# Kernel optimization log

Measured on AMD Instinct MI355X. Metric: run time of the kernel, lower is better.

## Reference

```python
import jax, jax.numpy as jnp
import numpy as np

N = 49152   # nodes (1024 graphs * 48 teeth)
G = 1024    # graphs
E = 65536   # edges per relation
H, C, R = 8, 48, 3
FUSED = 384
NEG = 0.2   # RGATConv negative_slope default
EPS = 1e-5


def _ln_global(x, w, b):
    # PyG LayerNorm mode='graph' with batch=None: normalize over ALL elements
    x = x - jnp.mean(x)
    return x / (jnp.std(x) + EPS) * w + b


def _ln_graph(x, batch, w, b):
    # PyG LayerNorm mode='graph' with batch: per-graph mean/var over nodes+features
    f = x.shape[-1]
    cnt = jnp.maximum(jax.ops.segment_sum(jnp.ones((x.shape[0],), x.dtype), batch, num_segments=G), 1.0) * f
    mean = jax.ops.segment_sum(x, batch, num_segments=G).sum(-1) / cnt  # [G]
    xc = x - mean[batch][:, None]
    var = jax.ops.segment_sum(xc * xc, batch, num_segments=G).sum(-1) / cnt
    return xc / jnp.sqrt(var + EPS)[batch][:, None] * w + b


def _rgat(x, src, dst, etype, W, q, k, b):
    # RGATConv: per-relation transform, additive self-attention, across-relation segment softmax
    xt = jnp.einsum('nf,rfc->rnc', x, W)          # [R,N,H*C] transform once per relation
    oi = xt[etype, dst]                            # [E,H*C] destination (x_i) transformed
    oj = xt[etype, src]                            # [E,H*C] source (x_j) transformed
    alpha = jax.nn.leaky_relu(oi @ q + oj @ k, NEG)   # [E,H]
    m = jax.lax.stop_gradient(jax.ops.segment_max(alpha, dst, num_segments=N))
    a = jnp.exp(alpha - m[dst])
    s = jax.ops.segment_sum(a, dst, num_segments=N)
    a = a / (s[dst] + 1e-16)                       # segment softmax over in-edges per head
    msg = (a[:, :, None] * oj.reshape(-1, H, C)).reshape(-1, H * C)
    return jax.ops.segment_sum(msg, dst, num_segments=N) + b


def _enc(x, w, b, lw, lb):
    return _ln_global(jax.nn.relu(x @ w + b), lw, lb)


def _forward(floats, ei_o, ei_a, ei_s, batch):
    (x_visual, x_geom, x_prior, vis_w, vis_b, vis_lw, vis_lb, geom_w, geom_b, geom_lw, geom_lb,
     prior_w, prior_b, prior_lw, prior_lb, r1_w, r1_q, r1_k, r1_b, n1_w, n1_b,
     r2_w, r2_q, r2_k, r2_b, n2_w, n2_b, c_w1, c_b1, c_w2, c_b2) = floats
    ei = jnp.concatenate([ei_o, ei_a, ei_s], axis=1)
    etype = jnp.concatenate([jnp.zeros((ei_o.shape[1],), jnp.int32),
                             jnp.ones((ei_a.shape[1],), jnp.int32),
                             jnp.full((ei_s.shape[1],), 2, jnp.int32)])
    src, dst = ei[0], ei[1]
    h0 = jnp.concatenate([_enc(x_visual, vis_w, vis_b, vis_lw, vis_lb),
                          _enc(x_geom, geom_w, geom_b, geom_lw, geom_lb),
                          _enc(x_prior, prior_w, prior_b, prior_lw, prior_lb)], axis=-1)
    h1 = _ln_graph(h0 + jax.nn.elu(_rgat(h0, src, dst, etype, r1_w, r1_q, r1_k, r1_b)), batch, n1_w, n1_b)
    h2 = _ln_graph(h1 + jax.nn.elu(_rgat(h1, src, dst, etype, r2_w, r2_q, r2_k, r2_b)), batch, n2_w, n2_b)
    return jax.nn.relu(h2 @ c_w1 + c_b1) @ c_w2 + c_b2


def setup_inputs() -> dict:
    key = jax.random.key(0)
    ks = jax.random.split(key, 20)
    def rn(i, shape, s=0.05):
        return jax.random.normal(ks[i], shape, jnp.float32) * s
    return dict(
        x_visual=rn(0, (N, 1024), 1.0),
        x_geom=rn(1, (N, 6), 1.0),
        x_prior=rn(2, (N, 50), 1.0),
        vis_w=rn(3, (1024, 128)), vis_b=jnp.zeros((128,)), vis_lw=jnp.ones((128,)), vis_lb=jnp.zeros((128,)),
        geom_w=rn(4, (6, 128)), geom_b=jnp.zeros((128,)), geom_lw=jnp.ones((128,)), geom_lb=jnp.zeros((128,)),
        prior_w=rn(5, (50, 128)), prior_b=jnp.zeros((128,)), prior_lw=jnp.ones((128,)), prior_lb=jnp.zeros((128,)),
        r1_w=rn(6, (R, FUSED, H * C)), r1_q=rn(7, (H * C, H)), r1_k=rn(8, (H * C, H)), r1_b=jnp.zeros((H * C,)),
        n1_w=jnp.ones((FUSED,)), n1_b=jnp.zeros((FUSED,)),
        r2_w=rn(9, (R, FUSED, H * C)), r2_q=rn(10, (H * C, H)), r2_k=rn(11, (H * C, H)), r2_b=jnp.zeros((H * C,)),
        n2_w=jnp.ones((FUSED,)), n2_b=jnp.zeros((FUSED,)),
        c_w1=rn(12, (FUSED, 128)), c_b1=jnp.zeros((128,)), c_w2=rn(13, (128, 49)), c_b2=jnp.zeros((49,)),
        edge_index_overlap=jax.random.randint(ks[14], (2, E), 0, N),
        edge_index_arch=jax.random.randint(ks[15], (2, E), 0, N),
        edge_index_spatial=jax.random.randint(ks[16], (2, E), 0, N),
        batch=jnp.sort(jax.random.randint(ks[17], (N,), 0, G)),
    )


def reference(x_visual, x_geom, x_prior, vis_w, vis_b, vis_lw, vis_lb, geom_w, geom_b, geom_lw, geom_lb, prior_w, prior_b, prior_lw, prior_lb, r1_w, r1_q, r1_k, r1_b, n1_w, n1_b, r2_w, r2_q, r2_k, r2_b, n2_w, n2_b, c_w1, c_b1, c_w2, c_b2, edge_index_overlap, edge_index_arch, edge_index_spatial, batch):
    floats = (x_visual, x_geom, x_prior, vis_w, vis_b, vis_lw, vis_lb, geom_w, geom_b, geom_lw, geom_lb,
              prior_w, prior_b, prior_lw, prior_lb, r1_w, r1_q, r1_k, r1_b, n1_w, n1_b,
              r2_w, r2_q, r2_k, r2_b, n2_w, n2_b, c_w1, c_b1, c_w2, c_b2)
    return _forward(floats, edge_index_overlap, edge_index_arch, edge_index_spatial, batch)
```

## Files before the change

### kernel.cpp

```cpp
#include <hip/hip_runtime.h>
#include <hip/hip_bf16.h>

#define NN 49152
#define GG 1024
#define EE 65536
#define ETOT 196608
#define FF 384
#define NEG_SLOPE 0.2f

typedef __attribute__((ext_vector_type(8))) short bf16x8;
typedef __attribute__((ext_vector_type(4))) float f32x4;

__device__ __forceinline__ float wave_sum(float v) {
#pragma unroll
    for (int m = 32; m; m >>= 1) v += __shfl_xor(v, m);
    return v;
}
__device__ __forceinline__ unsigned short f2bf(float f) {
    __hip_bfloat16 b = __float2bfloat16(f);
    return *reinterpret_cast<unsigned short*>(&b);
}
__device__ __forceinline__ float bflo(unsigned u) { return __uint_as_float(u << 16); }
__device__ __forceinline__ float bfhi(unsigned u) { return __uint_as_float(u & 0xffff0000u); }
__device__ __forceinline__ unsigned pk2(float lo, float hi) {
    return ((unsigned)f2bf(hi) << 16) | (unsigned)f2bf(lo);
}

__device__ __forceinline__ void gload_lds16(const void* g, void* l) {
    __builtin_amdgcn_global_load_lds(
        (const __attribute__((address_space(1))) unsigned int*)g,
        (__attribute__((address_space(3))) unsigned int*)l, 16, 0, 0);
}

__device__ __forceinline__ int swz(int row, int c16) {
    return row * 64 + ((c16 ^ ((row >> 1) & 3)) << 4);
}

template <int ACT, bool ABF, bool OBF>
__global__ __launch_bounds__(256) void gemm_mfma(
    const void* __restrict__ Ag, int K,
    const unsigned short* __restrict__ Btg,
    const float* __restrict__ bias,
    void* __restrict__ Cg, int ldc,
    size_t bzs, size_t czs)
{
    __shared__ __align__(16) char As[8192];
    __shared__ __align__(16) char Bs[8192];
    const unsigned short* Bt = Btg + (size_t)blockIdx.z * bzs;
    int t = threadIdx.x;
    int bm = blockIdx.x << 7, bn = blockIdx.y << 7;
    int lane = t & 63, wid = t >> 6, wr = wid >> 1, wc = wid & 1;
    f32x4 acc[4][4] = {};
    int ktn = K >> 5;
    for (int kt = 0; kt < ktn; ++kt) {
        int k0 = kt << 5;
#pragma unroll
        for (int ii = 0; ii < 2; ++ii) {
            int id = t + (ii << 8);
            int row = id >> 2, c = id & 3;
            int csrc = c ^ ((row >> 1) & 3);
            size_t ldsoff = (size_t)((wid << 10) + (ii << 12));
            if (ABF) {
                const unsigned short* srcA = (const unsigned short*)Ag + (size_t)(bm + row) * K + k0 + csrc * 8;
                gload_lds16(srcA, As + ldsoff);
            } else {
                const float* srcA = (const float*)Ag + (size_t)(bm + row) * K + k0 + c * 8;
                float4 a0 = *(const float4*)srcA;
                float4 a1 = *(const float4*)(srcA + 4);
                union { unsigned short u[8]; int4 v; } P;
                P.u[0] = f2bf(a0.x); P.u[1] = f2bf(a0.y); P.u[2] = f2bf(a0.z); P.u[3] = f2bf(a0.w);
                P.u[4] = f2bf(a1.x); P.u[5] = f2bf(a1.y); P.u[6] = f2bf(a1.z); P.u[7] = f2bf(a1.w);
                *(int4*)(As + swz(row, c)) = P.v;
            }
            const unsigned short* srcB = Bt + (size_t)(bn + row) * K + k0 + csrc * 8;
            gload_lds16(srcB, Bs + ldsoff);
        }
        __syncthreads();
        int c16 = lane >> 4;
        bf16x8 af[4], bfr[4];
#pragma unroll
        for (int m = 0; m < 4; ++m)
            af[m] = *(const bf16x8*)(As + swz((wr << 6) + (m << 4) + (lane & 15), c16));
#pragma unroll
        for (int n = 0; n < 4; ++n)
            bfr[n] = *(const bf16x8*)(Bs + swz((wc << 6) + (n << 4) + (lane & 15), c16));
#pragma unroll
        for (int m = 0; m < 4; ++m)
#pragma unroll
            for (int n = 0; n < 4; ++n)
                acc[m][n] = __builtin_amdgcn_mfma_f32_16x16x32_bf16(af[m], bfr[n], acc[m][n], 0, 0, 0);
        __syncthreads();
    }
#pragma unroll
    for (int m = 0; m < 4; ++m) {
#pragma unroll
        for (int n = 0; n < 4; ++n) {
            int row0 = bm + (wr << 6) + (m << 4) + ((lane >> 4) << 2);
            int col = bn + (wc << 6) + (n << 4) + (lane & 15);
            float bv = bias ? bias[col] : 0.f;
#pragma unroll
            for (int j = 0; j < 4; ++j) {
                float v = acc[m][n][j] + bv;
                if (ACT == 1) v = fmaxf(v, 0.f);
                if (OBF) {
                    unsigned short* C = (unsigned short*)Cg + (size_t)blockIdx.z * czs;
                    C[(size_t)(row0 + j) * ldc + col] = f2bf(v);
                } else {
                    float* C = (float*)Cg + (size_t)blockIdx.z * czs;
                    C[(size_t)(row0 + j) * ldc + col] = v;
                }
            }
        }
    }
}

template <int ACT, bool OBF>
__global__ __launch_bounds__(256) void gemm_k(
    const float* __restrict__ A, int K,
    const float* __restrict__ W, int Jw,
    const float* __restrict__ bias,
    void* __restrict__ Cg, int ldc, int jmax)
{
    __shared__ float Ash[16][64];
    __shared__ float Bsh[16][68];
    int tid = threadIdx.x;
    int bj = blockIdx.x << 6;
    int bm = blockIdx.y << 6;
    int tx = tid & 15, ty = tid >> 4;
    float acc[4][4] = {};
    int ktn = (K + 15) >> 4;
    int ar = tid >> 2;
    int aks = (tid & 3) << 2;
    int wk = tid >> 4;
    int wjs = (tid & 15) << 2;
    for (int kt = 0; kt < ktn; ++kt) {
        int k0 = kt << 4;
        const float* Ap = A + (size_t)(bm + ar) * K + k0 + aks;
#pragma unroll
        for (int i = 0; i < 4; ++i) {
            int k = k0 + aks + i;
            Ash[aks + i][ar] = (k < K) ? Ap[i] : 0.f;
        }
        const float* Wp = W + (size_t)(k0 + wk) * Jw + bj + wjs;
        bool kok = (k0 + wk) < K;
#pragma unroll
        for (int i = 0; i < 4; ++i) {
            int j = bj + wjs + i;
            Bsh[wk][wjs + i] = (kok && j < jmax) ? Wp[i] : 0.f;
        }
        __syncthreads();
#pragma unroll
        for (int kk = 0; kk < 16; ++kk) {
            const float4 av = *reinterpret_cast<const float4*>(&Ash[kk][ty << 2]);
            const float4 bv = *reinterpret_cast<const float4*>(&Bsh[kk][tx << 2]);
            float aa[4] = {av.x, av.y, av.z, av.w};
            float bb[4] = {bv.x, bv.y, bv.z, bv.w};
#pragma unroll
            for (int i = 0; i < 4; ++i)
#pragma unroll
                for (int j = 0; j < 4; ++j)
                    acc[i][j] = fmaf(aa[i], bb[j], acc[i][j]);
        }
        __syncthreads();
    }
#pragma unroll
    for (int i = 0; i < 4; ++i) {
        int row = bm + (ty << 2) + i;
#pragma unroll
        for (int j = 0; j < 4; ++j) {
            int col = bj + (tx << 2) + j;
            if (col < jmax) {
                float v = acc[i][j];
                if (bias) v += bias[col];
                if (ACT == 1) v = fmaxf(v, 0.f);
                if (OBF) ((unsigned short*)Cg)[(size_t)row * ldc + col] = f2bf(v);
                else     ((float*)Cg)[(size_t)row * ldc + col] = v;
            }
        }
    }
}

__global__ void transpose_bf(const float* __restrict__ W, unsigned short* __restrict__ Wt,
                             int K, int N, int total) {
    int i = blockIdx.x * 256 + threadIdx.x;
    if (i >= total) return;
    int kn = K * N;
    int z = i / kn, rem = i - z * kn;
    int k = rem / N, n = rem - k * N;
    Wt[(size_t)z * kn + (size_t)n * K + k] = f2bf(W[i]);
}

__global__ void transpose2_bf(const float* __restrict__ W1, const float* __restrict__ W2,
                              unsigned short* __restrict__ Wt1, unsigned short* __restrict__ Wt2) {
    int i = blockIdx.x * 256 + threadIdx.x;
    if (i >= 6 * FF * FF) return;
    int z = i / (FF * FF), rem = i - z * (FF * FF);
    int k = rem / FF, n = rem - k * FF;
    const float* W = (z < 3) ? W1 + (size_t)z * FF * FF : W2 + (size_t)(z - 3) * FF * FF;
    unsigned short* Wt = (z < 3) ? Wt1 + (size_t)z * FF * FF : Wt2 + (size_t)(z - 3) * FF * FF;
    Wt[(size_t)n * FF + k] = f2bf(W[(size_t)k * FF + n]);
}

__global__ __launch_bounds__(256) void wqk_prep2(
    const float* __restrict__ rw1, const float* __restrict__ q1, const float* __restrict__ k1,
    const float* __restrict__ rw2, const float* __restrict__ q2, const float* __restrict__ k2,
    unsigned short* __restrict__ wqkt1, unsigned short* __restrict__ wqkt2)
{
    __shared__ float qsT[16 * 384];
    int t = threadIdx.x;
    int r = blockIdx.x, ftile = blockIdx.y, layer = blockIdx.z;
    const float* rw = layer ? rw2 : rw1;
    const float* q = layer ? q2 : q1;
    const float* k = layer ? k2 : k1;
    unsigned short* wqkt = layer ? wqkt2 : wqkt1;
    for (int idx = t; idx < 384 * 16; idx += 256) {
        int c = idx >> 4, j = idx & 15;
        qsT[j * 384 + c] = (j < 8) ? q[c * 8 + j] : k[c * 8 + j - 8];
    }
    __syncthreads();
    int j = t & 15, fi = t >> 4;
    const float4* q4 = (const float4*)(qsT + j * 384);
#pragma unroll
    for (int rr = 0; rr < 4; ++rr) {
        int f = ftile * 64 + fi * 4 + rr;
        const float4* a4 = (const float4*)(rw + (size_t)r * FF * FF + (size_t)f * FF);
        float dot = 0.f;
        for (int c4 = 0; c4 < 96; ++c4) {
            float4 a = a4[c4], b = q4[c4];
            dot += a.x * b.x + a.y * b.y + a.z * b.z + a.w * b.w;
        }
        wqkt[(size_t)(r * 16 + j) * FF + f] = f2bf(dot);
    }
}

__global__ void csr_count(const int* __restrict__ eo, const int* __restrict__ ea,
                          const int* __restrict__ es, int* __restrict__ deg) {
    int e = blockIdx.x * 256 + threadIdx.x;
    if (e >= ETOT) return;
    int et = e >> 16, le = e & 65535;
    const int* ei = et == 0 ? eo : (et == 1 ? ea : es);
    atomicAdd(&deg[ei[EE + le]], 1);
}
__global__ void csr_alloc(const int* __restrict__ deg, int* __restrict__ counter,
                          int* __restrict__ rps, const int* __restrict__ batch,
                          float* __restrict__ gcnt) {
    int n = blockIdx.x * 256 + threadIdx.x;
    int lane = threadIdx.x & 63;
    int d = (n < NN) ? deg[n] : 0;
    int x = d;
#pragma unroll
    for (int off = 1; off < 64; off <<= 1) {
        int y = __shfl_up(x, off);
        if (lane >= off) x += y;
    }
    int total = __shfl(x, 63);
    int base = 0;
    if (lane == 63) base = atomicAdd(counter, total);
    base = __shfl(base, 63);
    if (n < NN) {
        rps[n] = base + x - d;
        atomicAdd(&gcnt[batch[n]], 1.f);
    }
}
__global__ void csr_fill(const int* __restrict__ eo, const int* __restrict__ ea,
                         const int* __restrict__ es, const int* __restrict__ rps,
                         int* __restrict__ fill, int* __restrict__ elist) {
    int e = blockIdx.x * 256 + threadIdx.x;
    if (e >= ETOT) return;
    int et = e >> 16, le = e & 65535;
    const int* ei = et == 0 ? eo : (et == 1 ? ea : es);
    int src = ei[le], dst = ei[EE + le];
    int pos = rps[dst] + atomicAdd(&fill[dst], 1);
    elist[pos] = (et << 16) | src;
}

#define ERB 512
__global__ __launch_bounds__(256) void enc_reduce_stage1(const unsigned short* __restrict__ hb, float* __restrict__ pbuf) {
    __shared__ float part[4][6];
    float a1 = 0.f, a2 = 0.f, b1 = 0.f, b2 = 0.f, c1 = 0.f, c2 = 0.f;
    const uint4* h8 = (const uint4*)hb;
    int total8 = NN * FF / 8;
    for (int i = blockIdx.x * 256 + threadIdx.x; i < total8; i += ERB * 256) {
        uint4 v = h8[i];
        float e0 = bflo(v.x), e1 = bfhi(v.x), e2 = bflo(v.y), e3 = bfhi(v.y);
        float e4 = bflo(v.z), e5 = bfhi(v.z), e6 = bflo(v.w), e7 = bfhi(v.w);
        float s1 = e0 + e1 + e2 + e3 + e4 + e5 + e6 + e7;
        float s2 = e0*e0 + e1*e1 + e2*e2 + e3*e3 + e4*e4 + e5*e5 + e6*e6 + e7*e7;
        int enc = (i % 48) >> 4;
        if (enc == 0)      { a1 += s1; a2 += s2; }
        else if (enc == 1) { b1 += s1; b2 += s2; }
        else               { c1 += s1; c2 += s2; }
    }
    a1 = wave_sum(a1); a2 = wave_sum(a2);
    b1 = wave_sum(b1); b2 = wave_sum(b2);
    c1 = wave_sum(c1); c2 = wave_sum(c2);
    int w = threadIdx.x >> 6;
    if ((threadIdx.x & 63) == 0) {
        part[w][0] = a1; part[w][1] = a2; part[w][2] = b1;
        part[w][3] = b2; part[w][4] = c1; part[w][5] = c2;
    }
    __syncthreads();
    if (threadIdx.x < 6) {
        float s = part[0][threadIdx.x] + part[1][threadIdx.x] + part[2][threadIdx.x] + part[3][threadIdx.x];
        pbuf[blockIdx.x * 6 + threadIdx.x] = s;
    }
}

__global__ void enc_reduce_stage2(const float* __restrict__ pbuf, float* __restrict__ est) {
    int lane = threadIdx.x;
    float s[6] = {};
    for (int b = lane; b < ERB; b += 64)
#pragma unroll
        for (int j = 0; j < 6; ++j) s[j] += pbuf[b * 6 + j];
#pragma unroll
    for (int j = 0; j < 6; ++j) {
        float v = wave_sum(s[j]);
        if (lane == 0) est[j] = v;
    }
    __syncthreads();
    if (lane < 3) {
        float cnt = (float)NN * 128.f;
        float mean = est[2 * lane] / cnt;
        float var = est[2 * lane + 1] / cnt - mean * mean;
        var = fmaxf(var, 0.f);
        est[6 + 2 * lane] = mean;
        est[7 + 2 * lane] = 1.f / (sqrtf(var) + 1e-5f);
    }
}

__global__ __launch_bounds__(256) void enc_apply(
    unsigned short* __restrict__ hb, const float* __restrict__ est,
    const float* __restrict__ lw0, const float* __restrict__ lb0,
    const float* __restrict__ lw1, const float* __restrict__ lb1,
    const float* __restrict__ lw2, const float* __restrict__ lb2)
{
    long gt = (long)blockIdx.x * 256 + threadIdx.x;
    if (gt >= (long)NN * FF) return;
    int f = (int)(gt % FF);
    int enc = f >> 7, j = f & 127;
    const float* lw = enc == 0 ? lw0 : (enc == 1 ? lw1 : lw2);
    const float* lb = enc == 0 ? lb0 : (enc == 1 ? lb1 : lb2);
    float mean = est[6 + 2 * enc], sc = est[7 + 2 * enc];
    float v = (bflo((unsigned)hb[gt]) - mean) * sc * lw[j] + lb[j];
    hb[gt] = f2bf(v);
}

__global__ __launch_bounds__(256) void qk48_mfma(
    const unsigned short* __restrict__ hb,
    const unsigned short* __restrict__ wqkt,
    float* __restrict__ qkbuf)
{
    __shared__ __align__(16) unsigned short wlds[48 * 392];
    int t = threadIdx.x;
    for (int idx = t; idx < 48 * 192; idx += 256) {
        int row = idx / 192, dw = idx - row * 192;
        *((unsigned*)(wlds + row * 392) + dw) = ((const unsigned*)wqkt)[row * 192 + dw];
    }
    __syncthreads();
    int lane = t & 63, wid = t >> 6;
    int col = lane & 15, kq = lane >> 4;
    int tile = blockIdx.x * 4 + wid;
    const unsigned short* arow = hb + (size_t)(tile * 16 + col) * FF + kq * 8;
    f32x4 acc0 = {}, acc1 = {}, acc2 = {};
#pragma unroll
    for (int kt = 0; kt < 12; ++kt) {
        bf16x8 af = *(const bf16x8*)(arow + kt * 32);
        bf16x8 b0 = *(const bf16x8*)(wlds + (0 * 16 + col) * 392 + kt * 32 + kq * 8);
        bf16x8 b1 = *(const bf16x8*)(wlds + (1 * 16 + col) * 392 + kt * 32 + kq * 8);
        bf16x8 b2 = *(const bf16x8*)(wlds + (2 * 16 + col) * 392 + kt * 32 + kq * 8);
        acc0 = __builtin_amdgcn_mfma_f32_16x16x32_bf16(af, b0, acc0, 0, 0, 0);
        acc1 = __builtin_amdgcn_mfma_f32_16x16x32_bf16(af, b1, acc1, 0, 0, 0);
        acc2 = __builtin_amdgcn_mfma_f32_16x16x32_bf16(af, b2, acc2, 0, 0, 0);
    }
    int row0 = kq << 2;
#pragma unroll
    for (int j = 0; j < 4; ++j) {
        size_t node = (size_t)tile * 16 + row0 + j;
        qkbuf[node * 48 + 0 + col]  = acc0[j];
        qkbuf[node * 48 + 16 + col] = acc1[j];
        qkbuf[node * 48 + 32 + col] = acc2[j];
    }
}

__global__ __launch_bounds__(256) void gather_fused(
    const int* __restrict__ rps, const int* __restrict__ deg, const int* __restrict__ elist,
    const float* __restrict__ qkbuf, const unsigned short* __restrict__ xt,
    const unsigned short* __restrict__ hbin, const float* __restrict__ rb, const int* __restrict__ batch,
    float* __restrict__ gs1, float* __restrict__ gs2, unsigned short* __restrict__ ybuf)
{
    int node = blockIdx.x * 4 + (threadIdx.x >> 6);
    int lane = threadIdx.x & 63;
    int d = deg[node], rp = rps[node];
    int head = lane >> 3;
    float qd0 = qkbuf[(size_t)node * 48 + 0 + head];
    float qd1 = qkbuf[(size_t)node * 48 + 16 + head];
    float qd2 = qkbuf[(size_t)node * 48 + 32 + head];
    const unsigned* hr = (const unsigned*)(hbin + (size_t)node * FF) + lane * 3;
    unsigned h0u = hr[0], h1u = hr[1], h2u = hr[2];
    float s = 0.f;
    float acc0 = 0.f, acc1 = 0.f, acc2 = 0.f, acc3 = 0.f, acc4 = 0.f, acc5 = 0.f;
    for (int base = 0; base < d; base += 64) {
        int myp = (base + lane < d) ? elist[rp + base + lane] : 0;
        int lim = d - base; if (lim > 64) lim = 64;
        for (int e = 0; e < lim; ++e) {
            int packed = __shfl(myp, e);
            int et = packed >> 16, src = packed & 0xFFFF;
            const unsigned* xr = (const unsigned*)(xt + ((size_t)et * NN + src) * FF) + lane * 3;
            unsigned u0 = xr[0], u1 = xr[1], u2 = xr[2];
            float qd = et == 0 ? qd0 : (et == 1 ? qd1 : qd2);
            float a = qd + qkbuf[(size_t)src * 48 + et * 16 + 8 + head];
            a = a >= 0.f ? a : NEG_SLOPE * a;
            float pw = __expf(a);
            s += pw;
            acc0 = fmaf(pw, bflo(u0), acc0); acc1 = fmaf(pw, bfhi(u0), acc1);
            acc2 = fmaf(pw, bflo(u1), acc2); acc3 = fmaf(pw, bfhi(u1), acc3);
            acc4 = fmaf(pw, bflo(u2), acc4); acc5 = fmaf(pw, bfhi(u2), acc5);
        }
    }
    float inv = 1.f / (s + 1e-16f);
    float hv[6] = {bflo(h0u), bfhi(h0u), bflo(h1u), bfhi(h1u), bflo(h2u), bfhi(h2u)};
    float av[6] = {acc0, acc1, acc2, acc3, acc4, acc5};
    int f0 = lane * 6;
    float s1 = 0.f, s2 = 0.f;
    float yv[6];
#pragma unroll
    for (int i = 0; i < 6; ++i) {
        float mv = av[i] * inv + rb[f0 + i];
        float e = mv > 0.f ? mv : (__expf(mv) - 1.f);
        float y = hv[i] + e;
        yv[i] = y;
        s1 += y; s2 += y * y;
    }
    unsigned* yrow = (unsigned*)(ybuf + (size_t)node * FF) + lane * 3;
    yrow[0] = pk2(yv[0], yv[1]);
    yrow[1] = pk2(yv[2], yv[3]);
    yrow[2] = pk2(yv[4], yv[5]);
    s1 = wave_sum(s1);
    s2 = wave_sum(s2);
    if (lane == 0) {
        int g = batch[node];
        atomicAdd(&gs1[g], s1);
        atomicAdd(&gs2[g], s2);
    }
}

__global__ __launch_bounds__(256) void ln_apply(
    const unsigned short* __restrict__ y, const int* __restrict__ batch,
    const float* __restrict__ gcnt, const float* __restrict__ gs1, const float* __restrict__ gs2,
    const float* __restrict__ w, const float* __restrict__ b,
    unsigned short* __restrict__ hbOut)
{
    long gt = (long)blockIdx.x * 256 + threadIdx.x;
    int n = (int)(gt >> 6);
    if (n >= NN) return;
    int lane = (int)(gt & 63);
    int f0 = lane * 6;
    int g = batch[n];
    float cnt = fmaxf(gcnt[g], 1.f) * (float)FF;
    float mean = gs1[g] / cnt;
    float var = fmaxf(gs2[g] / cnt - mean * mean, 0.f);
    float rs = 1.f / sqrtf(var + 1e-5f);
    const unsigned* yr = (const unsigned*)(y + (size_t)n * FF) + lane * 3;
    unsigned u0 = yr[0], u1 = yr[1], u2 = yr[2];
    float yv[6] = {bflo(u0), bfhi(u0), bflo(u1), bfhi(u1), bflo(u2), bfhi(u2)};
    float ov[6];
#pragma unroll
    for (int i = 0; i < 6; ++i)
        ov[i] = (yv[i] - mean) * rs * w[f0 + i] + b[f0 + i];
    unsigned* orow = (unsigned*)(hbOut + (size_t)n * FF) + lane * 3;
    orow[0] = pk2(ov[0], ov[1]);
    orow[1] = pk2(ov[2], ov[3]);
    orow[2] = pk2(ov[4], ov[5]);
}

static void rgat_layer(hipStream_t stream,
    const unsigned short* hbIn,
    const float* rb, const float* lnw, const float* lnb,
    const int* rps, const int* deg, const int* elist, const int* batch,
    const unsigned short* wt, unsigned short* xt, const unsigned short* wqkt, float* qkbuf,
    float* gs, const float* gcnt,
    unsigned short* ybuf, unsigned short* hbOut)
{
    gemm_mfma<0, true, true><<<dim3(384, 3, 3), 256, 0, stream>>>(
        hbIn, FF, wt, nullptr, xt, FF, (size_t)FF * FF, (size_t)NN * FF);
    qk48_mfma<<<NN / 64, 256, 0, stream>>>(hbIn, wqkt, qkbuf);
    gather_fused<<<NN / 4, 256, 0, stream>>>(rps, deg, elist, qkbuf, xt, hbIn, rb, batch,
                                             gs, gs + GG, ybuf);
    ln_apply<<<NN / 4, 256, 0, stream>>>(ybuf, batch, gcnt, gs, gs + GG, lnw, lnb, hbOut);
}

extern "C" void kernel_launch(void* const* d_in, const int* in_sizes, int n_in,
                              void* d_out, int out_size, void* d_ws, size_t ws_size,
                              hipStream_t stream)
{
    const float* x_visual = (const float*)d_in[0];
    const float* x_geom   = (const float*)d_in[1];
    const float* x_prior  = (const float*)d_in[2];
    const float* vis_w  = (const float*)d_in[3];
    const float* vis_b  = (const float*)d_in[4];
    const float* vis_lw = (const float*)d_in[5];
    const float* vis_lb = (const float*)d_in[6];
    const float* geom_w  = (const float*)d_in[7];
    const float* geom_b  = (const float*)d_in[8];
    const float* geom_lw = (const float*)d_in[9];
    const float* geom_lb = (const float*)d_in[10];
    const float* prior_w  = (const float*)d_in[11];
    const float* prior_b  = (const float*)d_in[12];
    const float* prior_lw = (const float*)d_in[13];
    const float* prior_lb = (const float*)d_in[14];
    const float* r1_w = (const float*)d_in[15];
    const float* r1_q = (const float*)d_in[16];
    const float* r1_k = (const float*)d_in[17];
    const float* r1_b = (const float*)d_in[18];
    const float* n1_w = (const float*)d_in[19];
    const float* n1_b = (const float*)d_in[20];
    const float* r2_w = (const float*)d_in[21];
    const float* r2_q = (const float*)d_in[22];
    const float* r2_k = (const float*)d_in[23];
    const float* r2_b = (const float*)d_in[24];
    const float* n2_w = (const float*)d_in[25];
    const float* n2_b = (const float*)d_in[26];
    const float* c_w1 = (const float*)d_in[27];
    const float* c_b1 = (const float*)d_in[28];
    const float* c_w2 = (const float*)d_in[29];
    const float* c_b2 = (const float*)d_in[30];
    const int* ei_o  = (const int*)d_in[31];
    const int* ei_a  = (const int*)d_in[32];
    const int* ei_s  = (const int*)d_in[33];
    const int* batch = (const int*)d_in[34];
    float* out = (float*)d_out;

    char* p = (char*)d_ws;
    auto alloc = [&](size_t bytes) { char* r = p; p += (bytes + 255) & ~(size_t)255; return r; };
    unsigned short* hbA = (unsigned short*)alloc((size_t)NN * FF * 2);
    unsigned short* hbB = (unsigned short*)alloc((size_t)NN * FF * 2);
    unsigned short* ybuf = (unsigned short*)alloc((size_t)NN * FF * 2);
    unsigned short* xt = (unsigned short*)alloc((size_t)3 * NN * FF * 2);
    unsigned short* wt1 = (unsigned short*)alloc((size_t)3 * FF * FF * 2);
    unsigned short* wt2 = (unsigned short*)alloc((size_t)3 * FF * FF * 2);
    unsigned short* wtv = (unsigned short*)alloc((size_t)1024 * 128 * 2);
    unsigned short* wtc = (unsigned short*)alloc((size_t)FF * 128 * 2);
    float* qkbuf = (float*)alloc((size_t)NN * 48 * 4);
    unsigned short* wqkt1 = (unsigned short*)alloc((size_t)48 * FF * 2);
    unsigned short* wqkt2 = (unsigned short*)alloc((size_t)48 * FF * 2);
    float* t128 = (float*)alloc((size_t)NN * 128 * 4);
    int* rps = (int*)alloc(NN * 4);
    int* elist = (int*)alloc(ETOT * 4);
    float* est = (float*)alloc(64);
    float* pbuf = (float*)alloc(ERB * 6 * 4);
    char* z0 = alloc((size_t)2 * NN * 4 + 256 + (size_t)4 * GG * 4 + GG * 4);
    int* deg = (int*)z0;
    int* fill = deg + NN;
    int* counter = (int*)(z0 + (size_t)2 * NN * 4);
    float* gs = (float*)(z0 + (size_t)2 * NN * 4 + 256);
    float* gcnt = gs + 4 * GG;
    hipMemsetAsync(z0, 0, (size_t)2 * NN * 4 + 256 + (size_t)4 * GG * 4 + GG * 4, stream);

    csr_count<<<ETOT / 256, 256, 0, stream>>>(ei_o, ei_a, ei_s, deg);
    csr_alloc<<<NN / 256, 256, 0, stream>>>(deg, counter, rps, batch, gcnt);
    csr_fill<<<ETOT / 256, 256, 0, stream>>>(ei_o, ei_a, ei_s, rps, fill, elist);

    transpose2_bf<<<(6 * FF * FF + 255) / 256, 256, 0, stream>>>(r1_w, r2_w, wt1, wt2);
    wqk_prep2<<<dim3(3, 6, 2), 256, 0, stream>>>(r1_w, r1_q, r1_k, r2_w, r2_q, r2_k, wqkt1, wqkt2);
    transpose_bf<<<(1024 * 128 + 255) / 256, 256, 0, stream>>>(vis_w, wtv, 1024, 128, 1024 * 128);
    transpose_bf<<<(FF * 128 + 255) / 256, 256, 0, stream>>>(c_w1, wtc, FF, 128, FF * 128);

    gemm_mfma<1, false, true><<<dim3(384, 1, 1), 256, 0, stream>>>(
        x_visual, 1024, wtv, vis_b, hbA, FF, 0, 0);
    gemm_k<1, true><<<dim3(2, 768, 1), 256, 0, stream>>>(x_geom, 6, geom_w, 128, geom_b, hbA + 128, FF, 128);
    gemm_k<1, true><<<dim3(2, 768, 1), 256, 0, stream>>>(x_prior, 50, prior_w, 128, prior_b, hbA + 256, FF, 128);
    enc_reduce_stage1<<<ERB, 256, 0, stream>>>(hbA, pbuf);
    enc_reduce_stage2<<<1, 64, 0, stream>>>(pbuf, est);
    enc_apply<<<(int)((size_t)NN * FF / 256), 256, 0, stream>>>(
        hbA, est, vis_lw, vis_lb, geom_lw, geom_lb, prior_lw, prior_lb);

    rgat_layer(stream, hbA, r1_b, n1_w, n1_b, rps, deg, elist, batch,
               wt1, xt, wqkt1, qkbuf, gs, gcnt, ybuf, hbB);
    rgat_layer(stream, hbB, r2_b, n2_w, n2_b, rps, deg, elist, batch,
               wt2, xt, wqkt2, qkbuf, gs + 2 * GG, gcnt, ybuf, hbA);

    gemm_mfma<1, true, false><<<dim3(384, 1, 1), 256, 0, stream>>>(
        hbA, FF, wtc, c_b1, t128, 128, 0, 0);
    gemm_k<0, false><<<dim3(1, 768, 1), 256, 0, stream>>>(t128, 128, c_w2, 49, c_b2, out, 49, 49);
}
```

Before: 700.6 us.

## Widen gather loads to 16-byte vectors and merge geom/prior encoder GEMMs

The RGAT gather kernel now has 48 of 64 lanes each load 8 bf16 values (uint4) per edge row instead of 64 lanes loading 6 values through three 4-byte loads, which cuts the number of load instructions per gathered row. The head index changes to lane/6 so each lane still maps to the right attention head. Separately, the geom and prior encoder GEMMs are fused into one launch over blockIdx.z, removing one kernel launch. The trade-off is 16 idle lanes per wave in the gather loop.

Measured after the change: 678.7 us. 1.03x faster.

```diff
diff --git a/kernel.cpp b/kernel.cpp
--- a/kernel.cpp
+++ b/kernel.cpp
@@ -180,6 +180,69 @@
     }
 }
 
+__global__ __launch_bounds__(256) void gemm_k2_enc(
+    const float* __restrict__ A0, const float* __restrict__ W0, const float* __restrict__ b0,
+    const float* __restrict__ A1, const float* __restrict__ W1, const float* __restrict__ b1,
+    unsigned short* __restrict__ hb)
+{
+    __shared__ float Ash[16][64];
+    __shared__ float Bsh[16][68];
+    int z = blockIdx.z;
+    const float* A = z ? A1 : A0;
+    const float* W = z ? W1 : W0;
+    const float* bias = z ? b1 : b0;
+    int K = z ? 50 : 6;
+    int colbase = z ? 256 : 128;
+    int tid = threadIdx.x;
+    int bj = blockIdx.x << 6;
+    int bm = blockIdx.y << 6;
+    int tx = tid & 15, ty = tid >> 4;
+    float acc[4][4] = {};
+    int ktn = (K + 15) >> 4;
+    int ar = tid >> 2;
+    int aks = (tid & 3) << 2;
+    int wk = tid >> 4;
+    int wjs = (tid & 15) << 2;
+    for (int kt = 0; kt < ktn; ++kt) {
+        int k0 = kt << 4;
+        const float* Ap = A + (size_t)(bm + ar) * K + k0 + aks;
+#pragma unroll
+        for (int i = 0; i < 4; ++i) {
+            int k = k0 + aks + i;
+            Ash[aks + i][ar] = (k < K) ? Ap[i] : 0.f;
+        }
+        const float* Wp = W + (size_t)(k0 + wk) * 128 + bj + wjs;
+        bool kok = (k0 + wk) < K;
+#pragma unroll
+        for (int i = 0; i < 4; ++i)
+            Bsh[wk][wjs + i] = kok ? Wp[i] : 0.f;
+        __syncthreads();
+#pragma unroll
+        for (int kk = 0; kk < 16; ++kk) {
+            const float4 av = *reinterpret_cast<const float4*>(&Ash[kk][ty << 2]);
+            const float4 bv = *reinterpret_cast<const float4*>(&Bsh[kk][tx << 2]);
+            float aa[4] = {av.x, av.y, av.z, av.w};
+            float bb[4] = {bv.x, bv.y, bv.z, bv.w};
+#pragma unroll
+            for (int i = 0; i < 4; ++i)
+#pragma unroll
+                for (int j = 0; j < 4; ++j)
+                    acc[i][j] = fmaf(aa[i], bb[j], acc[i][j]);
+        }
+        __syncthreads();
+    }
+#pragma unroll
+    for (int i = 0; i < 4; ++i) {
+        int row = bm + (ty << 2) + i;
+#pragma unroll
+        for (int j = 0; j < 4; ++j) {
+            int col = bj + (tx << 2) + j;
+            float v = fmaxf(acc[i][j] + bias[col], 0.f);
+            hb[(size_t)row * FF + colbase + col] = f2bf(v);
+        }
+    }
+}
+
 __global__ void transpose_bf(const float* __restrict__ W, unsigned short* __restrict__ Wt,
                              int K, int N, int total) {
     int i = blockIdx.x * 256 + threadIdx.x;
@@ -390,51 +453,56 @@
 {
     int node = blockIdx.x * 4 + (threadIdx.x >> 6);
     int lane = threadIdx.x & 63;
+    bool act = lane < 48;
     int d = deg[node], rp = rps[node];
-    int head = lane >> 3;
+    int head = lane / 6; if (head > 7) head = 7;
     float qd0 = qkbuf[(size_t)node * 48 + 0 + head];
     float qd1 = qkbuf[(size_t)node * 48 + 16 + head];
     float qd2 = qkbuf[(size_t)node * 48 + 32 + head];
-    const unsigned* hr = (const unsigned*)(hbin + (size_t)node * FF) + lane * 3;
-    unsigned h0u = hr[0], h1u = hr[1], h2u = hr[2];
+    uint4 hu = {0, 0, 0, 0};
+    if (act) hu = *((const uint4*)(hbin + (size_t)node * FF) + lane);
     float s = 0.f;
-    float acc0 = 0.f, acc1 = 0.f, acc2 = 0.f, acc3 = 0.f, acc4 = 0.f, acc5 = 0.f;
+    float a0 = 0.f, a1 = 0.f, a2 = 0.f, a3 = 0.f, a4 = 0.f, a5 = 0.f, a6 = 0.f, a7 = 0.f;
     for (int base = 0; base < d; base += 64) {
         int myp = (base + lane < d) ? elist[rp + base + lane] : 0;
         int lim = d - base; if (lim > 64) lim = 64;
         for (int e = 0; e < lim; ++e) {
             int packed = __shfl(myp, e);
             int et = packed >> 16, src = packed & 0xFFFF;
-            const unsigned* xr = (const unsigned*)(xt + ((size_t)et * NN + src) * FF) + lane * 3;
-            unsigned u0 = xr[0], u1 = xr[1], u2 = xr[2];
+            uint4 u = {0, 0, 0, 0};
+            if (act) u = *((const uint4*)(xt + ((size_t)et * NN + src) * FF) + lane);
             float qd = et == 0 ? qd0 : (et == 1 ? qd1 : qd2);
             float a = qd + qkbuf[(size_t)src * 48 + et * 16 + 8 + head];
             a = a >= 0.f ? a : NEG_SLOPE * a;
             float pw = __expf(a);
             s += pw;
-            acc0 = fmaf(pw, bflo(u0), acc0); acc1 = fmaf(pw, bfhi(u0), acc1);
-            acc2 = fmaf(pw, bflo(u1), acc2); acc3 = fmaf(pw, bfhi(u1), acc3);
-            acc4 = fmaf(pw, bflo(u2), acc4); acc5 = fmaf(pw, bfhi(u2), acc5);
+            a0 = fmaf(pw, bflo(u.x), a0); a1 = fmaf(pw, bfhi(u.x), a1);
+            a2 = fmaf(pw, bflo(u.y), a2); a3 = fmaf(pw, bfhi(u.y), a3);
+            a4 = fmaf(pw, bflo(u.z), a4); a5 = fmaf(pw, bfhi(u.z), a5);
+            a6 = fmaf(pw, bflo(u.w), a6); a7 = fmaf(pw, bfhi(u.w), a7);
         }
     }
     float inv = 1.f / (s + 1e-16f);
-    float hv[6] = {bflo(h0u), bfhi(h0u), bflo(h1u), bfhi(h1u), bflo(h2u), bfhi(h2u)};
-    float av[6] = {acc0, acc1, acc2, acc3, acc4, acc5};
-    int f0 = lane * 6;
+    float hv[8] = {bflo(hu.x), bfhi(hu.x), bflo(hu.y), bfhi(hu.y),
+                   bflo(hu.z), bfhi(hu.z), bflo(hu.w), bfhi(hu.w)};
+    float av[8] = {a0, a1, a2, a3, a4, a5, a6, a7};
+    int f0 = lane * 8;
     float s1 = 0.f, s2 = 0.f;
-    float yv[6];
-#pragma unroll
-    for (int i = 0; i < 6; ++i) {
-        float mv = av[i] * inv + rb[f0 + i];
-        float e = mv > 0.f ? mv : (__expf(mv) - 1.f);
-        float y = hv[i] + e;
-        yv[i] = y;
-        s1 += y; s2 += y * y;
-    }
-    unsigned* yrow = (unsigned*)(ybuf + (size_t)node * FF) + lane * 3;
-    yrow[0] = pk2(yv[0], yv[1]);
-    yrow[1] = pk2(yv[2], yv[3]);
-    yrow[2] = pk2(yv[4], yv[5]);
+    if (act) {
+        float yv[8];
+#pragma unroll
+        for (int i = 0; i < 8; ++i) {
+            float mv = av[i] * inv + rb[f0 + i];
+            float e = mv > 0.f ? mv : (__expf(mv) - 1.f);
+            float y = hv[i] + e;
+            yv[i] = y;
+            s1 += y; s2 += y * y;
+        }
+        uint4 pkv;
+        pkv.x = pk2(yv[0], yv[1]); pkv.y = pk2(yv[2], yv[3]);
+        pkv.z = pk2(yv[4], yv[5]); pkv.w = pk2(yv[6], yv[7]);
+        *((uint4*)(ybuf + (size_t)node * FF) + lane) = pkv;
+    }
     s1 = wave_sum(s1);
     s2 = wave_sum(s2);
     if (lane == 0) {
@@ -567,8 +635,8 @@
 
     gemm_mfma<1, false, true><<<dim3(384, 1, 1), 256, 0, stream>>>(
         x_visual, 1024, wtv, vis_b, hbA, FF, 0, 0);
-    gemm_k<1, true><<<dim3(2, 768, 1), 256, 0, stream>>>(x_geom, 6, geom_w, 128, geom_b, hbA + 128, FF, 128);
-    gemm_k<1, true><<<dim3(2, 768, 1), 256, 0, stream>>>(x_prior, 50, prior_w, 128, prior_b, hbA + 256, FF, 128);
+    gemm_k2_enc<<<dim3(2, 768, 2), 256, 0, stream>>>(
+        x_geom, geom_w, geom_b, x_prior, prior_w, prior_b, hbA);
     enc_reduce_stage1<<<ERB, 256, 0, stream>>>(hbA, pbuf);
     enc_reduce_stage2<<<1, 64, 0, stream>>>(pbuf, est);
     enc_apply<<<(int)((size_t)NN * FF / 256), 256, 0, stream>>>(
```
